# Performance work log

Measured on AMD Instinct MI355X. Metric: run time of the kernel, lower is better.

## Reference

```python
import jax, jax.numpy as jnp
import numpy as np

N = 50000
E = 800000
D_IN = 128
D_HID = 256


def setup_inputs() -> dict:
    key = jax.random.key(0)
    ks = jax.random.split(key, 12)
    s = 0.02
    return {
        "node_features": jax.random.normal(ks[0], (N, D_IN), dtype=jnp.float32),
        "edge_index": jax.random.randint(ks[1], (2, E), 0, N, dtype=jnp.int64),
        # layer 0 (input_dim -> hidden)
        "eps0": jnp.zeros((), dtype=jnp.float32),
        "W1_0": jax.random.normal(ks[2], (D_IN, D_HID), dtype=jnp.float32) * s,
        "b1_0": jnp.zeros((D_HID,), dtype=jnp.float32),
        "W2_0": jax.random.normal(ks[3], (D_HID, D_HID), dtype=jnp.float32) * s,
        "b2_0": jnp.zeros((D_HID,), dtype=jnp.float32),
        # layer 1 (hidden -> hidden)
        "eps1": jnp.zeros((), dtype=jnp.float32),
        "W1_1": jax.random.normal(ks[4], (D_HID, D_HID), dtype=jnp.float32) * s,
        "b1_1": jnp.zeros((D_HID,), dtype=jnp.float32),
        "W2_1": jax.random.normal(ks[5], (D_HID, D_HID), dtype=jnp.float32) * s,
        "b2_1": jnp.zeros((D_HID,), dtype=jnp.float32),
        # fc_out (hidden -> input_dim)
        "Wo": jax.random.normal(ks[6], (D_HID, D_IN), dtype=jnp.float32) * s,
        "bo": jnp.zeros((D_IN,), dtype=jnp.float32),
    }


def _gin_layer(x, src, dst, eps, W1, b1, W2, b2):
    # gather neighbor features + scatter-add into destination nodes
    agg = jnp.zeros_like(x).at[dst].add(x[src])  # [N, d]
    h = (1.0 + eps) * x + agg
    h = jax.nn.relu(h @ W1 + b1)
    return h @ W2 + b2


def reference(node_features, edge_index, eps0, W1_0, b1_0, W2_0, b2_0,
              eps1, W1_1, b1_1, W2_1, b2_1, Wo, bo):
    src, dst = edge_index[0], edge_index[1]
    h = _gin_layer(node_features, src, dst, eps0, W1_0, b1_0, W2_0, b2_0)
    h = _gin_layer(h, src, dst, eps1, W1_1, b1_1, W2_1, b2_1)
    return h @ Wo + bo  # [N, input_dim]
```

## Files before the change

kernel.cpp:

```cpp
#include <hip/hip_runtime.h>

#define NN 50000
#define NE 800000
#define DIN 128
#define DHID 256
#define MAXDEG 128

typedef __bf16 bf16x8 __attribute__((ext_vector_type(8)));
typedef float f32x4 __attribute__((ext_vector_type(4)));

static __device__ __forceinline__ unsigned short f2bf(float f) {
    unsigned u = __float_as_uint(f);
    unsigned r = 0x7fffu + ((u >> 16) & 1u);
    return (unsigned short)((u + r) >> 16);
}
static __device__ __forceinline__ float blo(unsigned u) { return __uint_as_float(u << 16); }
static __device__ __forceinline__ float bhi(unsigned u) { return __uint_as_float(u & 0xffff0000u); }


__global__ void bucket_kernel(const int* __restrict__ src, const int* __restrict__ dst,
                              int* __restrict__ cnt, int* __restrict__ srcs, int E) {
    int i8 = (blockIdx.x * blockDim.x + threadIdx.x) * 8;
    if (i8 >= E) return;
    int4 da = *(const int4*)&dst[i8];
    int4 db = *(const int4*)&dst[i8 + 4];
    int4 sa = *(const int4*)&src[i8];
    int4 sb = *(const int4*)&src[i8 + 4];
    int t0 = atomicAdd(&cnt[da.x], 1);
    int t1 = atomicAdd(&cnt[da.y], 1);
    int t2 = atomicAdd(&cnt[da.z], 1);
    int t3 = atomicAdd(&cnt[da.w], 1);
    int t4 = atomicAdd(&cnt[db.x], 1);
    int t5 = atomicAdd(&cnt[db.y], 1);
    int t6 = atomicAdd(&cnt[db.z], 1);
    int t7 = atomicAdd(&cnt[db.w], 1);
    if (t0 < MAXDEG) srcs[(size_t)da.x * MAXDEG + t0] = sa.x;
    if (t1 < MAXDEG) srcs[(size_t)da.y * MAXDEG + t1] = sa.y;
    if (t2 < MAXDEG) srcs[(size_t)da.z * MAXDEG + t2] = sa.z;
    if (t3 < MAXDEG) srcs[(size_t)da.w * MAXDEG + t3] = sa.w;
    if (t4 < MAXDEG) srcs[(size_t)db.x * MAXDEG + t4] = sb.x;
    if (t5 < MAXDEG) srcs[(size_t)db.y * MAXDEG + t5] = sb.y;
    if (t6 < MAXDEG) srcs[(size_t)db.z * MAXDEG + t6] = sb.z;
    if (t7 < MAXDEG) srcs[(size_t)db.w * MAXDEG + t7] = sb.w;
}


__global__ void prep_kernel(const float* __restrict__ x, unsigned short* __restrict__ xb,
                            int* __restrict__ cnt,
                            const float* __restrict__ W1_0, const float* __restrict__ W2_0,
                            const float* __restrict__ W1_1, const float* __restrict__ W2_1,
                            const float* __restrict__ Wo,
                            unsigned short* __restrict__ w10t, unsigned short* __restrict__ w20t,
                            unsigned short* __restrict__ w11t, unsigned short* __restrict__ w21t,
                            unsigned short* __restrict__ wot) {
    int i = blockIdx.x * blockDim.x + threadIdx.x;
    if (i < NN) cnt[i] = 0;
    if (i < 262144) {
        const float* W; unsigned short* Wt; int K, N, idx;
        if (i < 32768)        { W = W1_0; Wt = w10t; K = 128; N = 256; idx = i; }
        else if (i < 98304)   { W = W2_0; Wt = w20t; K = 256; N = 256; idx = i - 32768; }
        else if (i < 163840)  { W = W1_1; Wt = w11t; K = 256; N = 256; idx = i - 98304; }
        else if (i < 229376)  { W = W2_1; Wt = w21t; K = 256; N = 256; idx = i - 163840; }
        else                  { W = Wo;   Wt = wot;  K = 256; N = 128; idx = i - 229376; }
        int k = idx / N;
        int n = idx - k * N;
        Wt[(size_t)n * K + k] = f2bf(W[idx]);
    }
    if (i * 4 < NN * DIN) {
        float4 v = *(const float4*)(x + (size_t)i * 4);
        ushort4 o;
        o.x = f2bf(v.x); o.y = f2bf(v.y); o.z = f2bf(v.z); o.w = f2bf(v.w);
        *(ushort4*)(xb + (size_t)i * 4) = o;
    }
}


template <int D>
__global__ void agg_bf16_kernel(const unsigned short* __restrict__ x, const int* __restrict__ cnt,
                                const int* __restrict__ srcs, const float* __restrict__ eps_p,
                                unsigned short* __restrict__ out, int n) {
    constexpr int G = (D == 128) ? 4 : 2;
    constexpr int L = 64 / G;
    constexpr int RQ = D / 8;
    int tid = blockIdx.x * blockDim.x + threadIdx.x;
    int wid = tid >> 6;
    int lane = threadIdx.x & 63;
    int group = lane / L;
    int li = lane % L;
    int node = wid * G + group;
    if (node >= n) return;
    int deg = cnt[node]; if (deg > MAXDEG) deg = MAXDEG;
    const int* sp = srcs + (size_t)node * MAXDEG;
    const uint4* xp = (const uint4*)x;
    float e = 1.0f + eps_p[0];

    float a[8], b[8];
    #pragma unroll
    for (int j = 0; j < 8; j++) { a[j] = 0.f; b[j] = 0.f; }

    int i = 0;
    for (; i + 8 <= deg; i += 8) {
        int4 s0 = *(const int4*)&sp[i];
        int4 s1 = *(const int4*)&sp[i + 4];
        uint4 v0 = xp[(size_t)s0.x * RQ + li];
        uint4 v1 = xp[(size_t)s0.y * RQ + li];
        uint4 v2 = xp[(size_t)s0.z * RQ + li];
        uint4 v3 = xp[(size_t)s0.w * RQ + li];
        uint4 v4 = xp[(size_t)s1.x * RQ + li];
        uint4 v5 = xp[(size_t)s1.y * RQ + li];
        uint4 v6 = xp[(size_t)s1.z * RQ + li];
        uint4 v7 = xp[(size_t)s1.w * RQ + li];
        a[0] += blo(v0.x); a[1] += bhi(v0.x); a[2] += blo(v0.y); a[3] += bhi(v0.y);
        a[4] += blo(v0.z); a[5] += bhi(v0.z); a[6] += blo(v0.w); a[7] += bhi(v0.w);
        b[0] += blo(v1.x); b[1] += bhi(v1.x); b[2] += blo(v1.y); b[3] += bhi(v1.y);
        b[4] += blo(v1.z); b[5] += bhi(v1.z); b[6] += blo(v1.w); b[7] += bhi(v1.w);
        a[0] += blo(v2.x); a[1] += bhi(v2.x); a[2] += blo(v2.y); a[3] += bhi(v2.y);
        a[4] += blo(v2.z); a[5] += bhi(v2.z); a[6] += blo(v2.w); a[7] += bhi(v2.w);
        b[0] += blo(v3.x); b[1] += bhi(v3.x); b[2] += blo(v3.y); b[3] += bhi(v3.y);
        b[4] += blo(v3.z); b[5] += bhi(v3.z); b[6] += blo(v3.w); b[7] += bhi(v3.w);
        a[0] += blo(v4.x); a[1] += bhi(v4.x); a[2] += blo(v4.y); a[3] += bhi(v4.y);
        a[4] += blo(v4.z); a[5] += bhi(v4.z); a[6] += blo(v4.w); a[7] += bhi(v4.w);
        b[0] += blo(v5.x); b[1] += bhi(v5.x); b[2] += blo(v5.y); b[3] += bhi(v5.y);
        b[4] += blo(v5.z); b[5] += bhi(v5.z); b[6] += blo(v5.w); b[7] += bhi(v5.w);
        a[0] += blo(v6.x); a[1] += bhi(v6.x); a[2] += blo(v6.y); a[3] += bhi(v6.y);
        a[4] += blo(v6.z); a[5] += bhi(v6.z); a[6] += blo(v6.w); a[7] += bhi(v6.w);
        b[0] += blo(v7.x); b[1] += bhi(v7.x); b[2] += blo(v7.y); b[3] += bhi(v7.y);
        b[4] += blo(v7.z); b[5] += bhi(v7.z); b[6] += blo(v7.w); b[7] += bhi(v7.w);
    }
    for (; i + 4 <= deg; i += 4) {
        int4 s = *(const int4*)&sp[i];
        uint4 v0 = xp[(size_t)s.x * RQ + li];
        uint4 v1 = xp[(size_t)s.y * RQ + li];
        uint4 v2 = xp[(size_t)s.z * RQ + li];
        uint4 v3 = xp[(size_t)s.w * RQ + li];
        a[0] += blo(v0.x); a[1] += bhi(v0.x); a[2] += blo(v0.y); a[3] += bhi(v0.y);
        a[4] += blo(v0.z); a[5] += bhi(v0.z); a[6] += blo(v0.w); a[7] += bhi(v0.w);
        b[0] += blo(v1.x); b[1] += bhi(v1.x); b[2] += blo(v1.y); b[3] += bhi(v1.y);
        b[4] += blo(v1.z); b[5] += bhi(v1.z); b[6] += blo(v1.w); b[7] += bhi(v1.w);
        a[0] += blo(v2.x); a[1] += bhi(v2.x); a[2] += blo(v2.y); a[3] += bhi(v2.y);
        a[4] += blo(v2.z); a[5] += bhi(v2.z); a[6] += blo(v2.w); a[7] += bhi(v2.w);
        b[0] += blo(v3.x); b[1] += bhi(v3.x); b[2] += blo(v3.y); b[3] += bhi(v3.y);
        b[4] += blo(v3.z); b[5] += bhi(v3.z); b[6] += blo(v3.w); b[7] += bhi(v3.w);
    }
    for (; i < deg; i++) {
        uint4 v = xp[(size_t)sp[i] * RQ + li];
        a[0] += blo(v.x); a[1] += bhi(v.x); a[2] += blo(v.y); a[3] += bhi(v.y);
        a[4] += blo(v.z); a[5] += bhi(v.z); a[6] += blo(v.w); a[7] += bhi(v.w);
    }
    uint4 xv = xp[(size_t)node * RQ + li];
    a[0] += b[0] + e * blo(xv.x); a[1] += b[1] + e * bhi(xv.x);
    a[2] += b[2] + e * blo(xv.y); a[3] += b[3] + e * bhi(xv.y);
    a[4] += b[4] + e * blo(xv.z); a[5] += b[5] + e * bhi(xv.z);
    a[6] += b[6] + e * blo(xv.w); a[7] += b[7] + e * bhi(xv.w);
    uint4 o;
    o.x = (unsigned)f2bf(a[0]) | ((unsigned)f2bf(a[1]) << 16);
    o.y = (unsigned)f2bf(a[2]) | ((unsigned)f2bf(a[3]) << 16);
    o.z = (unsigned)f2bf(a[4]) | ((unsigned)f2bf(a[5]) << 16);
    o.w = (unsigned)f2bf(a[6]) | ((unsigned)f2bf(a[7]) << 16);
    ((uint4*)out)[(size_t)node * RQ + li] = o;
}


template <int K1, int THREE>
__global__ __launch_bounds__(512) void mlp_fused(
        const unsigned short* __restrict__ A,
        const unsigned short* __restrict__ W1t, const float* __restrict__ b1,
        const unsigned short* __restrict__ W2t, const float* __restrict__ b2,
        const unsigned short* __restrict__ W3t, const float* __restrict__ b3,
        unsigned short* __restrict__ Cb, float* __restrict__ Cf, int M) {
    constexpr int NKS1 = K1 / 32;
    __shared__ __align__(16) unsigned short H[64 * 256];

    const int lane = threadIdx.x & 63;
    const int w = threadIdx.x >> 6;
    const int quad = lane >> 4;
    const int l16 = lane & 15;
    const size_t rowbase = (size_t)blockIdx.x * 64;

    f32x4 acc[4][2];

    #pragma unroll
    for (int j = 0; j < 4; j++)
        #pragma unroll
        for (int nt = 0; nt < 2; nt++) acc[j][nt] = (f32x4)(0.f);
    #pragma unroll 2
    for (int ks = 0; ks < NKS1; ks++) {
        bf16x8 bw[2];
        #pragma unroll
        for (int nt = 0; nt < 2; nt++)
            bw[nt] = *(const bf16x8*)&W1t[(size_t)(w * 32 + nt * 16 + l16) * K1 + ks * 32 + quad * 8];
        #pragma unroll
        for (int j = 0; j < 4; j++) {
            bf16x8 af = *(const bf16x8*)&A[(rowbase + j * 16 + l16) * K1 + ks * 32 + quad * 8];
            #pragma unroll
            for (int nt = 0; nt < 2; nt++)
                acc[j][nt] = __builtin_amdgcn_mfma_f32_16x16x32_bf16(bw[nt], af, acc[j][nt], 0, 0, 0);
        }
    }
    {
        f32x4 bvv[2];
        #pragma unroll
        for (int nt = 0; nt < 2; nt++)
            bvv[nt] = *(const f32x4*)&b1[w * 32 + nt * 16 + quad * 4];
        #pragma unroll
        for (int j = 0; j < 4; j++) {
            int r = j * 16 + l16;
            #pragma unroll
            for (int nt = 0; nt < 2; nt++) {
                f32x4 v = acc[j][nt] + bvv[nt];
                v[0] = fmaxf(v[0], 0.f); v[1] = fmaxf(v[1], 0.f);
                v[2] = fmaxf(v[2], 0.f); v[3] = fmaxf(v[3], 0.f);
                int c = w * 4 + nt * 2 + (quad >> 1);
                int cs = c ^ (r & 7);
                uint2 o;
                o.x = (unsigned)f2bf(v[0]) | ((unsigned)f2bf(v[1]) << 16);
                o.y = (unsigned)f2bf(v[2]) | ((unsigned)f2bf(v[3]) << 16);
                *(uint2*)&H[r * 256 + cs * 8 + (quad & 1) * 4] = o;
            }
        }
    }
    __syncthreads();

    #pragma unroll
    for (int j = 0; j < 4; j++)
        #pragma unroll
        for (int nt = 0; nt < 2; nt++) acc[j][nt] = (f32x4)(0.f);
    #pragma unroll 2
    for (int ks = 0; ks < 8; ks++) {
        bf16x8 bw[2];
        #pragma unroll
        for (int nt = 0; nt < 2; nt++)
            bw[nt] = *(const bf16x8*)&W2t[(size_t)(w * 32 + nt * 16 + l16) * 256 + ks * 32 + quad * 8];
        #pragma unroll
        for (int j = 0; j < 4; j++) {
            int r = j * 16 + l16;
            int cs = (ks * 4 + quad) ^ (r & 7);
            bf16x8 af = *(const bf16x8*)&H[r * 256 + cs * 8];
            #pragma unroll
            for (int nt = 0; nt < 2; nt++)
                acc[j][nt] = __builtin_amdgcn_mfma_f32_16x16x32_bf16(bw[nt], af, acc[j][nt], 0, 0, 0);
        }
    }
    {
        f32x4 bvv[2];
        #pragma unroll
        for (int nt = 0; nt < 2; nt++)
            bvv[nt] = *(const f32x4*)&b2[w * 32 + nt * 16 + quad * 4];
        if constexpr (!THREE) {
            #pragma unroll
            for (int j = 0; j < 4; j++) {
                size_t gm = rowbase + j * 16 + l16;
                if (gm < (size_t)M) {
                    #pragma unroll
                    for (int nt = 0; nt < 2; nt++) {
                        f32x4 v = acc[j][nt] + bvv[nt];
                        uint2 o;
                        o.x = (unsigned)f2bf(v[0]) | ((unsigned)f2bf(v[1]) << 16);
                        o.y = (unsigned)f2bf(v[2]) | ((unsigned)f2bf(v[3]) << 16);
                        *(uint2*)&Cb[gm * 256 + w * 32 + nt * 16 + quad * 4] = o;
                    }
                }
            }
        } else {
            __syncthreads();
            #pragma unroll
            for (int j = 0; j < 4; j++) {
                int r = j * 16 + l16;
                #pragma unroll
                for (int nt = 0; nt < 2; nt++) {
                    f32x4 v = acc[j][nt] + bvv[nt];
                    int c = w * 4 + nt * 2 + (quad >> 1);
                    int cs = c ^ (r & 7);
                    uint2 o;
                    o.x = (unsigned)f2bf(v[0]) | ((unsigned)f2bf(v[1]) << 16);
                    o.y = (unsigned)f2bf(v[2]) | ((unsigned)f2bf(v[3]) << 16);
                    *(uint2*)&H[r * 256 + cs * 8 + (quad & 1) * 4] = o;
                }
            }
            __syncthreads();
        }
    }

    if constexpr (THREE) {
        f32x4 acc3[4];
        #pragma unroll
        for (int j = 0; j < 4; j++) acc3[j] = (f32x4)(0.f);
        #pragma unroll 2
        for (int ks = 0; ks < 8; ks++) {
            bf16x8 bw = *(const bf16x8*)&W3t[(size_t)(w * 16 + l16) * 256 + ks * 32 + quad * 8];
            #pragma unroll
            for (int j = 0; j < 4; j++) {
                int r = j * 16 + l16;
                int cs = (ks * 4 + quad) ^ (r & 7);
                bf16x8 af = *(const bf16x8*)&H[r * 256 + cs * 8];
                acc3[j] = __builtin_amdgcn_mfma_f32_16x16x32_bf16(bw, af, acc3[j], 0, 0, 0);
            }
        }
        f32x4 bv3 = *(const f32x4*)&b3[w * 16 + quad * 4];
        #pragma unroll
        for (int j = 0; j < 4; j++) {
            size_t gm = rowbase + j * 16 + l16;
            if (gm < (size_t)M) {
                f32x4 v = acc3[j] + bv3;
                *(f32x4*)&Cf[gm * 128 + w * 16 + quad * 4] = v;
            }
        }
    }
}


static inline size_t align256(size_t v) { return (v + 255) & ~(size_t)255; }

extern "C" void kernel_launch(void* const* d_in, const int* in_sizes, int n_in,
                              void* d_out, int out_size, void* d_ws, size_t ws_size,
                              hipStream_t stream) {
    const float* x        = (const float*)d_in[0];
    const int*   ei       = (const int*)d_in[1];
    const float* eps0     = (const float*)d_in[2];
    const float* W1_0     = (const float*)d_in[3];
    const float* b1_0     = (const float*)d_in[4];
    const float* W2_0     = (const float*)d_in[5];
    const float* b2_0     = (const float*)d_in[6];
    const float* eps1     = (const float*)d_in[7];
    const float* W1_1     = (const float*)d_in[8];
    const float* b1_1     = (const float*)d_in[9];
    const float* W2_1     = (const float*)d_in[10];
    const float* b2_1     = (const float*)d_in[11];
    const float* Wo       = (const float*)d_in[12];
    const float* bo       = (const float*)d_in[13];
    float* out            = (float*)d_out;

    const int* srcE = ei;
    const int* dstE = ei + NE;

    char* p = (char*)d_ws;
    size_t o = 0;
    int* cnt  = (int*)(p + o); o = align256(o + (size_t)NN * 4);
    int* srcs = (int*)(p + o); o = align256(o + (size_t)NN * MAXDEG * 4);
    unsigned short* xb   = (unsigned short*)(p + o); o = align256(o + (size_t)NN * DIN * 2);
    unsigned short* w10t = (unsigned short*)(p + o); o = align256(o + (size_t)DHID * DIN * 2);
    unsigned short* w20t = (unsigned short*)(p + o); o = align256(o + (size_t)DHID * DHID * 2);
    unsigned short* w11t = (unsigned short*)(p + o); o = align256(o + (size_t)DHID * DHID * 2);
    unsigned short* w21t = (unsigned short*)(p + o); o = align256(o + (size_t)DHID * DHID * 2);
    unsigned short* wot  = (unsigned short*)(p + o); o = align256(o + (size_t)DIN * DHID * 2);
    unsigned short* bufA = (unsigned short*)(p + o); o = align256(o + (size_t)NN * DHID * 2 + 65536);
    unsigned short* bufB = (unsigned short*)(p + o); o = align256(o + (size_t)NN * DHID * 2 + 65536);

    prep_kernel<<<(NN * DIN / 4 + 255) / 256, 256, 0, stream>>>(
        x, xb, cnt, W1_0, W2_0, W1_1, W2_1, Wo, w10t, w20t, w11t, w21t, wot);
    bucket_kernel<<<(NE / 8 + 255) / 256, 256, 0, stream>>>(srcE, dstE, cnt, srcs, NE);

    int aggBlocks128 = ((NN + 3) / 4 + 3) / 4;
    int aggBlocks256 = ((NN + 1) / 2 + 3) / 4;
    int mlpBlocks = (NN + 63) / 64;

    agg_bf16_kernel<DIN><<<aggBlocks128, 256, 0, stream>>>(xb, cnt, srcs, eps0, bufA, NN);
    mlp_fused<128, 0><<<mlpBlocks, 512, 0, stream>>>(
        bufA, w10t, b1_0, w20t, b2_0, nullptr, nullptr, bufB, nullptr, NN);

    agg_bf16_kernel<DHID><<<aggBlocks256, 256, 0, stream>>>(bufB, cnt, srcs, eps1, bufA, NN);
    mlp_fused<256, 1><<<mlpBlocks, 512, 0, stream>>>(
        bufA, w11t, b1_1, w21t, b2_1, wot, bo, nullptr, out, NN);
}
```

Before: 348.1 us.

## Fuse neighbor aggregation into MLP kernel via shared-memory staging

Removes the separate aggregation kernels and performs the gather-sum of neighbor features inside the fused MLP kernel. Each block aggregates its 64 rows into a swizzled shared-memory tile, and the first GEMM then reads its A operand from LDS instead of global memory. This saves the global write and re-read of the aggregated buffer plus two kernel launches. The cost is that the gather phase and the MFMA phase in a block are now serialized behind a barrier, and the 512-thread blocks with a large LDS tile may give less latency hiding for the irregular gathers.

```diff
diff --git a/kernel.cpp b/kernel.cpp
--- a/kernel.cpp
+++ b/kernel.cpp
@@ -75,100 +75,19 @@
 }
 
 
-template <int D>
-__global__ void agg_bf16_kernel(const unsigned short* __restrict__ x, const int* __restrict__ cnt,
-                                const int* __restrict__ srcs, const float* __restrict__ eps_p,
-                                unsigned short* __restrict__ out, int n) {
-    constexpr int G = (D == 128) ? 4 : 2;
-    constexpr int L = 64 / G;
-    constexpr int RQ = D / 8;
-    int tid = blockIdx.x * blockDim.x + threadIdx.x;
-    int wid = tid >> 6;
-    int lane = threadIdx.x & 63;
-    int group = lane / L;
-    int li = lane % L;
-    int node = wid * G + group;
-    if (node >= n) return;
-    int deg = cnt[node]; if (deg > MAXDEG) deg = MAXDEG;
-    const int* sp = srcs + (size_t)node * MAXDEG;
-    const uint4* xp = (const uint4*)x;
-    float e = 1.0f + eps_p[0];
-
-    float a[8], b[8];
-    #pragma unroll
-    for (int j = 0; j < 8; j++) { a[j] = 0.f; b[j] = 0.f; }
-
-    int i = 0;
-    for (; i + 8 <= deg; i += 8) {
-        int4 s0 = *(const int4*)&sp[i];
-        int4 s1 = *(const int4*)&sp[i + 4];
-        uint4 v0 = xp[(size_t)s0.x * RQ + li];
-        uint4 v1 = xp[(size_t)s0.y * RQ + li];
-        uint4 v2 = xp[(size_t)s0.z * RQ + li];
-        uint4 v3 = xp[(size_t)s0.w * RQ + li];
-        uint4 v4 = xp[(size_t)s1.x * RQ + li];
-        uint4 v5 = xp[(size_t)s1.y * RQ + li];
-        uint4 v6 = xp[(size_t)s1.z * RQ + li];
-        uint4 v7 = xp[(size_t)s1.w * RQ + li];
-        a[0] += blo(v0.x); a[1] += bhi(v0.x); a[2] += blo(v0.y); a[3] += bhi(v0.y);
-        a[4] += blo(v0.z); a[5] += bhi(v0.z); a[6] += blo(v0.w); a[7] += bhi(v0.w);
-        b[0] += blo(v1.x); b[1] += bhi(v1.x); b[2] += blo(v1.y); b[3] += bhi(v1.y);
-        b[4] += blo(v1.z); b[5] += bhi(v1.z); b[6] += blo(v1.w); b[7] += bhi(v1.w);
-        a[0] += blo(v2.x); a[1] += bhi(v2.x); a[2] += blo(v2.y); a[3] += bhi(v2.y);
-        a[4] += blo(v2.z); a[5] += bhi(v2.z); a[6] += blo(v2.w); a[7] += bhi(v2.w);
-        b[0] += blo(v3.x); b[1] += bhi(v3.x); b[2] += blo(v3.y); b[3] += bhi(v3.y);
-        b[4] += blo(v3.z); b[5] += bhi(v3.z); b[6] += blo(v3.w); b[7] += bhi(v3.w);
-        a[0] += blo(v4.x); a[1] += bhi(v4.x); a[2] += blo(v4.y); a[3] += bhi(v4.y);
-        a[4] += blo(v4.z); a[5] += bhi(v4.z); a[6] += blo(v4.w); a[7] += bhi(v4.w);
-        b[0] += blo(v5.x); b[1] += bhi(v5.x); b[2] += blo(v5.y); b[3] += bhi(v5.y);
-        b[4] += blo(v5.z); b[5] += bhi(v5.z); b[6] += blo(v5.w); b[7] += bhi(v5.w);
-        a[0] += blo(v6.x); a[1] += bhi(v6.x); a[2] += blo(v6.y); a[3] += bhi(v6.y);
-        a[4] += blo(v6.z); a[5] += bhi(v6.z); a[6] += blo(v6.w); a[7] += bhi(v6.w);
-        b[0] += blo(v7.x); b[1] += bhi(v7.x); b[2] += blo(v7.y); b[3] += bhi(v7.y);
-        b[4] += blo(v7.z); b[5] += bhi(v7.z); b[6] += blo(v7.w); b[7] += bhi(v7.w);
-    }
-    for (; i + 4 <= deg; i += 4) {
-        int4 s = *(const int4*)&sp[i];
-        uint4 v0 = xp[(size_t)s.x * RQ + li];
-        uint4 v1 = xp[(size_t)s.y * RQ + li];
-        uint4 v2 = xp[(size_t)s.z * RQ + li];
-        uint4 v3 = xp[(size_t)s.w * RQ + li];
-        a[0] += blo(v0.x); a[1] += bhi(v0.x); a[2] += blo(v0.y); a[3] += bhi(v0.y);
-        a[4] += blo(v0.z); a[5] += bhi(v0.z); a[6] += blo(v0.w); a[7] += bhi(v0.w);
-        b[0] += blo(v1.x); b[1] += bhi(v1.x); b[2] += blo(v1.y); b[3] += bhi(v1.y);
-        b[4] += blo(v1.z); b[5] += bhi(v1.z); b[6] += blo(v1.w); b[7] += bhi(v1.w);
-        a[0] += blo(v2.x); a[1] += bhi(v2.x); a[2] += blo(v2.y); a[3] += bhi(v2.y);
-        a[4] += blo(v2.z); a[5] += bhi(v2.z); a[6] += blo(v2.w); a[7] += bhi(v2.w);
-        b[0] += blo(v3.x); b[1] += bhi(v3.x); b[2] += blo(v3.y); b[3] += bhi(v3.y);
-        b[4] += blo(v3.z); b[5] += bhi(v3.z); b[6] += blo(v3.w); b[7] += bhi(v3.w);
-    }
-    for (; i < deg; i++) {
-        uint4 v = xp[(size_t)sp[i] * RQ + li];
-        a[0] += blo(v.x); a[1] += bhi(v.x); a[2] += blo(v.y); a[3] += bhi(v.y);
-        a[4] += blo(v.z); a[5] += bhi(v.z); a[6] += blo(v.w); a[7] += bhi(v.w);
-    }
-    uint4 xv = xp[(size_t)node * RQ + li];
-    a[0] += b[0] + e * blo(xv.x); a[1] += b[1] + e * bhi(xv.x);
-    a[2] += b[2] + e * blo(xv.y); a[3] += b[3] + e * bhi(xv.y);
-    a[4] += b[4] + e * blo(xv.z); a[5] += b[5] + e * bhi(xv.z);
-    a[6] += b[6] + e * blo(xv.w); a[7] += b[7] + e * bhi(xv.w);
-    uint4 o;
-    o.x = (unsigned)f2bf(a[0]) | ((unsigned)f2bf(a[1]) << 16);
-    o.y = (unsigned)f2bf(a[2]) | ((unsigned)f2bf(a[3]) << 16);
-    o.z = (unsigned)f2bf(a[4]) | ((unsigned)f2bf(a[5]) << 16);
-    o.w = (unsigned)f2bf(a[6]) | ((unsigned)f2bf(a[7]) << 16);
-    ((uint4*)out)[(size_t)node * RQ + li] = o;
-}
-
-
 template <int K1, int THREE>
 __global__ __launch_bounds__(512) void mlp_fused(
-        const unsigned short* __restrict__ A,
+        const unsigned short* __restrict__ X,
+        const int* __restrict__ cnt, const int* __restrict__ srcs,
+        const float* __restrict__ eps_p,
         const unsigned short* __restrict__ W1t, const float* __restrict__ b1,
         const unsigned short* __restrict__ W2t, const float* __restrict__ b2,
         const unsigned short* __restrict__ W3t, const float* __restrict__ b3,
         unsigned short* __restrict__ Cb, float* __restrict__ Cf, int M) {
     constexpr int NKS1 = K1 / 32;
+    constexpr int G = (K1 == 128) ? 4 : 2;
+    constexpr int L = 64 / G;
+    constexpr int RQ = K1 / 8;
     __shared__ __align__(16) unsigned short H[64 * 256];
 
     const int lane = threadIdx.x & 63;
@@ -177,6 +96,87 @@
     const int l16 = lane & 15;
     const size_t rowbase = (size_t)blockIdx.x * 64;
 
+    {
+        const int group = lane / L;
+        const int li = lane % L;
+        const uint4* xp = (const uint4*)X;
+        const float e = 1.0f + eps_p[0];
+        #pragma unroll
+        for (int p = 0; p < 8 / G; p++) {
+            const int r = w * 8 + p * G + group;
+            const size_t node = rowbase + r;
+            if (node < (size_t)M) {
+                int deg = cnt[node]; if (deg > MAXDEG) deg = MAXDEG;
+                const int* sp = srcs + (size_t)node * MAXDEG;
+                float a[8], b[8];
+                #pragma unroll
+                for (int j = 0; j < 8; j++) { a[j] = 0.f; b[j] = 0.f; }
+                int i = 0;
+                for (; i + 8 <= deg; i += 8) {
+                    int4 s0 = *(const int4*)&sp[i];
+                    int4 s1 = *(const int4*)&sp[i + 4];
+                    uint4 v0 = xp[(size_t)s0.x * RQ + li];
+                    uint4 v1 = xp[(size_t)s0.y * RQ + li];
+                    uint4 v2 = xp[(size_t)s0.z * RQ + li];
+                    uint4 v3 = xp[(size_t)s0.w * RQ + li];
+                    uint4 v4 = xp[(size_t)s1.x * RQ + li];
+                    uint4 v5 = xp[(size_t)s1.y * RQ + li];
+                    uint4 v6 = xp[(size_t)s1.z * RQ + li];
+                    uint4 v7 = xp[(size_t)s1.w * RQ + li];
+                    a[0] += blo(v0.x); a[1] += bhi(v0.x); a[2] += blo(v0.y); a[3] += bhi(v0.y);
+                    a[4] += blo(v0.z); a[5] += bhi(v0.z); a[6] += blo(v0.w); a[7] += bhi(v0.w);
+                    b[0] += blo(v1.x); b[1] += bhi(v1.x); b[2] += blo(v1.y); b[3] += bhi(v1.y);
+                    b[4] += blo(v1.z); b[5] += bhi(v1.z); b[6] += blo(v1.w); b[7] += bhi(v1.w);
+                    a[0] += blo(v2.x); a[1] += bhi(v2.x); a[2] += blo(v2.y); a[3] += bhi(v2.y);
+                    a[4] += blo(v2.z); a[5] += bhi(v2.z); a[6] += blo(v2.w); a[7] += bhi(v2.w);
+                    b[0] += blo(v3.x); b[1] += bhi(v3.x); b[2] += blo(v3.y); b[3] += bhi(v3.y);
+                    b[4] += blo(v3.z); b[5] += bhi(v3.z); b[6] += blo(v3.w); b[7] += bhi(v3.w);
+                    a[0] += blo(v4.x); a[1] += bhi(v4.x); a[2] += blo(v4.y); a[3] += bhi(v4.y);
+                    a[4] += blo(v4.z); a[5] += bhi(v4.z); a[6] += blo(v4.w); a[7] += bhi(v4.w);
+                    b[0] += blo(v5.x); b[1] += bhi(v5.x); b[2] += blo(v5.y); b[3] += bhi(v5.y);
+                    b[4] += blo(v5.z); b[5] += bhi(v5.z); b[6] += blo(v5.w); b[7] += bhi(v5.w);
+                    a[0] += blo(v6.x); a[1] += bhi(v6.x); a[2] += blo(v6.y); a[3] += bhi(v6.y);
+                    a[4] += blo(v6.z); a[5] += bhi(v6.z); a[6] += blo(v6.w); a[7] += bhi(v6.w);
+                    b[0] += blo(v7.x); b[1] += bhi(v7.x); b[2] += blo(v7.y); b[3] += bhi(v7.y);
+                    b[4] += blo(v7.z); b[5] += bhi(v7.z); b[6] += blo(v7.w); b[7] += bhi(v7.w);
+                }
+                for (; i + 4 <= deg; i += 4) {
+                    int4 s = *(const int4*)&sp[i];
+                    uint4 v0 = xp[(size_t)s.x * RQ + li];
+                    uint4 v1 = xp[(size_t)s.y * RQ + li];
+                    uint4 v2 = xp[(size_t)s.z * RQ + li];
+                    uint4 v3 = xp[(size_t)s.w * RQ + li];
+                    a[0] += blo(v0.x); a[1] += bhi(v0.x); a[2] += blo(v0.y); a[3] += bhi(v0.y);
+                    a[4] += blo(v0.z); a[5] += bhi(v0.z); a[6] += blo(v0.w); a[7] += bhi(v0.w);
+                    b[0] += blo(v1.x); b[1] += bhi(v1.x); b[2] += blo(v1.y); b[3] += bhi(v1.y);
+                    b[4] += blo(v1.z); b[5] += bhi(v1.z); b[6] += blo(v1.w); b[7] += bhi(v1.w);
+                    a[0] += blo(v2.x); a[1] += bhi(v2.x); a[2] += blo(v2.y); a[3] += bhi(v2.y);
+                    a[4] += blo(v2.z); a[5] += bhi(v2.z); a[6] += blo(v2.w); a[7] += bhi(v2.w);
+                    b[0] += blo(v3.x); b[1] += bhi(v3.x); b[2] += blo(v3.y); b[3] += bhi(v3.y);
+                    b[4] += blo(v3.z); b[5] += bhi(v3.z); b[6] += blo(v3.w); b[7] += bhi(v3.w);
+                }
+                for (; i < deg; i++) {
+                    uint4 v = xp[(size_t)sp[i] * RQ + li];
+                    a[0] += blo(v.x); a[1] += bhi(v.x); a[2] += blo(v.y); a[3] += bhi(v.y);
+                    a[4] += blo(v.z); a[5] += bhi(v.z); a[6] += blo(v.w); a[7] += bhi(v.w);
+                }
+                uint4 xv = xp[(size_t)node * RQ + li];
+                a[0] += b[0] + e * blo(xv.x); a[1] += b[1] + e * bhi(xv.x);
+                a[2] += b[2] + e * blo(xv.y); a[3] += b[3] + e * bhi(xv.y);
+                a[4] += b[4] + e * blo(xv.z); a[5] += b[5] + e * bhi(xv.z);
+                a[6] += b[6] + e * blo(xv.w); a[7] += b[7] + e * bhi(xv.w);
+                uint4 o;
+                o.x = (unsigned)f2bf(a[0]) | ((unsigned)f2bf(a[1]) << 16);
+                o.y = (unsigned)f2bf(a[2]) | ((unsigned)f2bf(a[3]) << 16);
+                o.z = (unsigned)f2bf(a[4]) | ((unsigned)f2bf(a[5]) << 16);
+                o.w = (unsigned)f2bf(a[6]) | ((unsigned)f2bf(a[7]) << 16);
+                const int cs = li ^ (r & 7);
+                *(uint4*)&H[r * K1 + cs * 8] = o;
+            }
+        }
+    }
+    __syncthreads();
+
     f32x4 acc[4][2];
 
     #pragma unroll
@@ -191,12 +191,15 @@
             bw[nt] = *(const bf16x8*)&W1t[(size_t)(w * 32 + nt * 16 + l16) * K1 + ks * 32 + quad * 8];
         #pragma unroll
         for (int j = 0; j < 4; j++) {
-            bf16x8 af = *(const bf16x8*)&A[(rowbase + j * 16 + l16) * K1 + ks * 32 + quad * 8];
+            int r = j * 16 + l16;
+            int cs = (ks * 4 + quad) ^ (r & 7);
+            bf16x8 af = *(const bf16x8*)&H[r * K1 + cs * 8];
             #pragma unroll
             for (int nt = 0; nt < 2; nt++)
                 acc[j][nt] = __builtin_amdgcn_mfma_f32_16x16x32_bf16(bw[nt], af, acc[j][nt], 0, 0, 0);
         }
     }
+    __syncthreads();
     {
         f32x4 bvv[2];
         #pragma unroll
@@ -343,22 +346,17 @@
     unsigned short* w11t = (unsigned short*)(p + o); o = align256(o + (size_t)DHID * DHID * 2);
     unsigned short* w21t = (unsigned short*)(p + o); o = align256(o + (size_t)DHID * DHID * 2);
     unsigned short* wot  = (unsigned short*)(p + o); o = align256(o + (size_t)DIN * DHID * 2);
-    unsigned short* bufA = (unsigned short*)(p + o); o = align256(o + (size_t)NN * DHID * 2 + 65536);
-    unsigned short* bufB = (unsigned short*)(p + o); o = align256(o + (size_t)NN * DHID * 2 + 65536);
+    unsigned short* bufB = (unsigned short*)(p + o); o = align256(o + (size_t)NN * DHID * 2);
 
     prep_kernel<<<(NN * DIN / 4 + 255) / 256, 256, 0, stream>>>(
         x, xb, cnt, W1_0, W2_0, W1_1, W2_1, Wo, w10t, w20t, w11t, w21t, wot);
     bucket_kernel<<<(NE / 8 + 255) / 256, 256, 0, stream>>>(srcE, dstE, cnt, srcs, NE);
 
-    int aggBlocks128 = ((NN + 3) / 4 + 3) / 4;
-    int aggBlocks256 = ((NN + 1) / 2 + 3) / 4;
     int mlpBlocks = (NN + 63) / 64;
 
-    agg_bf16_kernel<DIN><<<aggBlocks128, 256, 0, stream>>>(xb, cnt, srcs, eps0, bufA, NN);
     mlp_fused<128, 0><<<mlpBlocks, 512, 0, stream>>>(
-        bufA, w10t, b1_0, w20t, b2_0, nullptr, nullptr, bufB, nullptr, NN);
-
-    agg_bf16_kernel<DHID><<<aggBlocks256, 256, 0, stream>>>(bufB, cnt, srcs, eps1, bufA, NN);
+        xb, cnt, srcs, eps0, w10t, b1_0, w20t, b2_0, nullptr, nullptr, bufB, nullptr, NN);
+
     mlp_fused<256, 1><<<mlpBlocks, 512, 0, stream>>>(
-        bufA, w11t, b1_1, w21t, b2_1, wot, bo, nullptr, out, NN);
-}
+        bufB, cnt, srcs, eps1, w11t, b1_1, w21t, b2_1, wot, bo, nullptr, out, NN);
+}
```

After: 306.3 us. 12.0% less time.
